# Performance work log

Hardware: AMD Instinct MI355X
Metric: run time of the kernel (lower is better)

## Reference

```python
import jax, jax.numpy as jnp
import numpy as np

B, N, K = 8, 2048, 20
EPS = 1e-5
GROUPS = 32


def setup_inputs() -> dict:
    key = jax.random.key(0)
    ks = jax.random.split(key, 10)
    f32 = jnp.float32
    def W(k_, o, c):
        return jax.random.normal(k_, (o, c), f32) * 0.1
    p = {}
    p["transpose_xyz"] = jax.random.normal(ks[0], (B, 3, N), f32)
    p["w1"] = W(ks[1], 64, 6);    p["g1"] = jnp.ones(64, f32);  p["b1"] = jnp.zeros(64, f32)
    p["w2"] = W(ks[2], 64, 128);  p["g2"] = jnp.ones(64, f32);  p["b2"] = jnp.zeros(64, f32)
    p["w3"] = W(ks[3], 128, 128); p["g3"] = jnp.ones(128, f32); p["b3"] = jnp.zeros(128, f32)
    p["w4"] = W(ks[4], 256, 256); p["g4"] = jnp.ones(256, f32); p["b4"] = jnp.zeros(256, f32)
    p["w5"] = W(ks[5], 512, 512); p["g5"] = jnp.ones(512, f32); p["b5"] = jnp.zeros(512, f32)
    p["wm1"] = W(ks[6], 512, 1536); p["bm1"] = jnp.zeros(512, f32); p["g6"] = jnp.ones(512, f32); p["b6"] = jnp.zeros(512, f32)
    p["wm2"] = W(ks[7], 256, 512);  p["bm2"] = jnp.zeros(256, f32); p["g7"] = jnp.ones(256, f32); p["b7"] = jnp.zeros(256, f32)
    p["wm3"] = W(ks[8], 128, 256);  p["bm3"] = jnp.zeros(128, f32); p["g8"] = jnp.ones(128, f32); p["b8"] = jnp.zeros(128, f32)
    return p


def _lrelu(x):
    return jnp.where(x >= 0, x, 0.2 * x)


def _bn2d(x, g, b):
    # training-mode BatchNorm2d: stats over (B, N, K) per channel, biased variance
    m = jnp.mean(x, axis=(0, 2, 3), keepdims=True)
    v = jnp.var(x, axis=(0, 2, 3), keepdims=True)
    return (x - m) * jax.lax.rsqrt(v + EPS) * g[None, :, None, None] + b[None, :, None, None]


def _gn(x, g, b):
    # GroupNorm over [B, C, L]
    Bx, C, L = x.shape
    xr = x.reshape(Bx, GROUPS, C // GROUPS, L)
    m = jnp.mean(xr, axis=(2, 3), keepdims=True)
    v = jnp.var(xr, axis=(2, 3), keepdims=True)
    xn = ((xr - m) * jax.lax.rsqrt(v + EPS)).reshape(Bx, C, L)
    return xn * g[None, :, None] + b[None, :, None]


def _graph_feature(x, k):
    # x: [B, C, N] -> edge features [B, 2C, N, k]
    xx = jnp.sum(x * x, axis=1)                       # [B, N]
    inner = jnp.einsum('bcn,bcm->bnm', x, x)          # [B, N, N]
    pd = 2.0 * inner - xx[:, :, None] - xx[:, None, :]  # negative sq distance
    idx = jax.lax.top_k(pd, k)[1]                     # [B, N, k] nearest (incl. self)
    xt = jnp.transpose(x, (0, 2, 1))                  # [B, N, C]
    nbr = jax.vmap(lambda a, i: a[i])(xt, idx)        # [B, N, k, C]
    ctr = jnp.broadcast_to(xt[:, :, None, :], nbr.shape)
    f = jnp.concatenate([nbr - ctr, ctr], axis=-1)    # [B, N, k, 2C]
    return jnp.transpose(f, (0, 3, 1, 2))


def _edge_block(x, w, g, b, k):
    f = _graph_feature(x, k)                          # [B, 2C, N, k]
    f = jnp.einsum('oc,bcnk->bonk', w, f)             # 1x1 conv2d, no bias
    f = _lrelu(_bn2d(f, g, b))
    return jnp.max(f, axis=-1)                        # [B, O, N]


def _forward(transpose_xyz, w1, g1, b1, w2, g2, b2, w3, g3, b3, w4, g4, b4,
             w5, g5, b5, wm1, bm1, g6, b6, wm2, bm2, g7, b7, wm3, bm3, g8, b8):
    x1 = _edge_block(transpose_xyz, w1, g1, b1, K)    # [B, 64, N]
    x2 = _edge_block(x1, w2, g2, b2, K)               # [B, 64, N]
    x3 = _edge_block(x2, w3, g3, b3, K)               # [B, 128, N]
    x4 = _edge_block(x3, w4, g4, b4, K)               # [B, 256, N]
    loc = jnp.concatenate([x1, x2, x3, x4], axis=1)   # [B, 512, N]
    h = _lrelu(_gn(jnp.einsum('oc,bcn->bon', w5, loc), g5, b5))  # [B, 512, N]
    glb = jnp.concatenate([jnp.max(h, axis=2), jnp.mean(h, axis=2)], axis=1)  # [B, 1024]
    Bx, _, Nx = loc.shape
    rep = jnp.broadcast_to(glb[:, :, None], (Bx, glb.shape[1], Nx))
    cat = jnp.concatenate([loc, rep], axis=1)         # [B, 1536, N]
    h = jax.nn.relu(_gn(jnp.einsum('oc,bcn->bon', wm1, cat) + bm1[None, :, None], g6, b6))
    h = jax.nn.relu(_gn(jnp.einsum('oc,bcn->bon', wm2, h) + bm2[None, :, None], g7, b7))
    h = jax.nn.relu(_gn(jnp.einsum('oc,bcn->bon', wm3, h) + bm3[None, :, None], g8, b8))
    return h                                          # [B, 128, N]


def reference(transpose_xyz, w1, g1, b1, w2, g2, b2, w3, g3, b3, w4, g4, b4,
              w5, g5, b5, wm1, bm1, g6, b6, wm2, bm2, g7, b7, wm3, bm3, g8, b8):
    return _forward(transpose_xyz, w1, g1, b1, w2, g2, b2, w3, g3, b3, w4, g4, b4,
                    w5, g5, b5, wm1, bm1, g6, b6, wm2, bm2, g7, b7, wm3, bm3, g8, b8)
```

## Files before the change

kernel.cpp:

```cpp
#include <hip/hip_runtime.h>

#define BATCH 8
#define NPTS  2048
#define KNN   20
#define NEG_INF_F (-3.402823466e38f)
#define NEG_INF_D (-1.7976931348623157e308)

__device__ __forceinline__ float fmul_(float a, float b){ return __fmul_rn(a,b); }
__device__ __forceinline__ float fadd_(float a, float b){ return __fadd_rn(a,b); }
__device__ __forceinline__ float fsub_(float a, float b){ return __fsub_rn(a,b); }

__global__ void k_transpose_in(const float* __restrict__ x, float* __restrict__ o) {
    int i = blockIdx.x * blockDim.x + threadIdx.x;
    if (i >= BATCH * 3 * NPTS) return;
    int b = i / (3 * NPTS); int r = i % (3 * NPTS); int c = r / NPTS; int n = r % NPTS;
    size_t row = (size_t)b * NPTS + n;
    o[row * 4 + c] = x[i];
    if (c == 0) o[row * 4 + 3] = 0.f;
}

__global__ void k_sumsq(const float* __restrict__ X, int ldx, int coff, int C,
                        float* __restrict__ xx) {
    int i = blockIdx.x * blockDim.x + threadIdx.x;
    if (i >= BATCH * NPTS) return;
    const float* p = X + (size_t)i * ldx + coff;
    float s = 0.f;
    for (int c = 0; c < C; ++c) s = fadd_(s, fmul_(p[c], p[c]));
    xx[i] = s;
}

__global__ __launch_bounds__(256) void k_pd(const float* __restrict__ Xb, int ldx, int coff, int C,
                                            const float* __restrict__ xxb, float* __restrict__ pd) {
    __shared__ float An[64][17];
    __shared__ float Am[64][17];
    int tx = threadIdx.x, ty = threadIdx.y, tid = ty * 16 + tx;
    int lrow = tid >> 2, lc4 = (tid & 3) << 2;
    int nB = blockIdx.y * 64, mB = blockIdx.x * 64;
    float acc[4][4] = {};
    for (int k0 = 0; k0 < C; k0 += 16) {
        #pragma unroll
        for (int j = 0; j < 4; ++j) {
            int kc = k0 + lc4 + j;
            An[lrow][lc4+j] = (kc < C) ? Xb[(size_t)(nB + lrow) * ldx + coff + kc] : 0.f;
            Am[lrow][lc4+j] = (kc < C) ? Xb[(size_t)(mB + lrow) * ldx + coff + kc] : 0.f;
        }
        __syncthreads();
        #pragma unroll
        for (int kk = 0; kk < 16; ++kk) {
            float a[4], w[4];
            #pragma unroll
            for (int i = 0; i < 4; ++i) a[i] = An[ty*4+i][kk];
            #pragma unroll
            for (int j = 0; j < 4; ++j) w[j] = Am[tx*4+j][kk];
            #pragma unroll
            for (int i = 0; i < 4; ++i)
                #pragma unroll
                for (int j = 0; j < 4; ++j)
                    acc[i][j] = fadd_(acc[i][j], fmul_(a[i], w[j]));
        }
        __syncthreads();
    }
    #pragma unroll
    for (int i = 0; i < 4; ++i) {
        int n = nB + ty*4 + i;
        float xn = xxb[n];
        #pragma unroll
        for (int j = 0; j < 4; ++j) {
            int m = mB + tx*4 + j;
            pd[(size_t)n * NPTS + m] = fsub_(fsub_(fmul_(2.0f, acc[i][j]), xn), xxb[m]);
        }
    }
}

__global__ __launch_bounds__(256) void k_topk(const float* __restrict__ pd, int gbase,
                                              int* __restrict__ idx) {
    __shared__ float wv_[4];
    __shared__ int   wi_[4];
    __shared__ int   gi_;
    int r = blockIdx.x, tid = threadIdx.x;
    const float* src = pd + (size_t)r * NPTS;
    float v[8];
    #pragma unroll
    for (int j = 0; j < 8; ++j) v[j] = src[tid + j * 256];
    float lv = v[0]; int lj = 0;
    #pragma unroll
    for (int j = 1; j < 8; ++j) if (v[j] > lv) { lv = v[j]; lj = j; }
    int lane = tid & 63, wid = tid >> 6;
    for (int it = 0; it < KNN; ++it) {
        float bv = lv; int bm = tid + lj * 256;
        #pragma unroll
        for (int d = 32; d > 0; d >>= 1) {
            float ov = __shfl_xor(bv, d, 64);
            int   om = __shfl_xor(bm, d, 64);
            if (ov > bv || (ov == bv && om < bm)) { bv = ov; bm = om; }
        }
        if (lane == 0) { wv_[wid] = bv; wi_[wid] = bm; }
        __syncthreads();
        if (tid == 0) {
            float gv = wv_[0]; int gm = wi_[0];
            #pragma unroll
            for (int k = 1; k < 4; ++k) {
                float ov = wv_[k]; int om = wi_[k];
                if (ov > gv || (ov == gv && om < gm)) { gv = ov; gm = om; }
            }
            gi_ = gm;
            idx[(size_t)(gbase + r) * KNN + it] = gm;
        }
        __syncthreads();
        int gm = gi_;
        if ((gm & 255) == tid) {
            v[gm >> 8] = NEG_INF_F;
            lv = v[0]; lj = 0;
            #pragma unroll
            for (int j = 1; j < 8; ++j) if (v[j] > lv) { lv = v[j]; lj = j; }
        }
    }
}

#define CCHUNK 16
__global__ void k_edge_conv(const float* __restrict__ X, int ldx, int coff, int C, int O,
                            const float* __restrict__ w, const int* __restrict__ idx,
                            float* __restrict__ ymax, double* __restrict__ part) {
    __shared__ float sc[128];
    __shared__ int   si[KNN];
    __shared__ float sn[KNN * 128];
    __shared__ float wt[256 * (CCHUNK + 1)];
    int o = threadIdx.x;
    int blk = blockIdx.x;
    int C2 = 2 * C;
    double s1 = 0.0, s2 = 0.0;
    for (int jn = 0; jn < 8; ++jn) {
        int n = blk * 8 + jn;
        int b = n >> 11, nl = n & 2047;
        const float* Xb = X + ((size_t)b * NPTS) * ldx + coff;
        for (int t = o; t < C; t += O) sc[t] = Xb[(size_t)nl * ldx + t];
        if (o < KNN) si[o] = idx[(size_t)n * KNN + o];
        __syncthreads();
        for (int t = o; t < KNN * C; t += O) sn[t] = Xb[(size_t)si[t / C] * ldx + (t % C)];
        __syncthreads();
        float acc[KNN];
        #pragma unroll
        for (int k = 0; k < KNN; ++k) acc[k] = 0.f;
        for (int c0 = 0; c0 < C2; c0 += CCHUNK) {
            for (int t = o; t < O * CCHUNK; t += O) {
                int oo = t / CCHUNK, c2 = t % CCHUNK; int c = c0 + c2;
                wt[oo * (CCHUNK + 1) + c2] = (c < C2) ? w[(size_t)oo * C2 + c] : 0.f;
            }
            __syncthreads();
            int cend = (C2 - c0 < CCHUNK) ? (C2 - c0) : CCHUNK;
            for (int c2 = 0; c2 < cend; ++c2) {
                int c = c0 + c2;
                float wv = wt[o * (CCHUNK + 1) + c2];
                if (c < C) {
                    float cv = sc[c];
                    #pragma unroll
                    for (int k = 0; k < KNN; ++k)
                        acc[k] = fadd_(acc[k], fmul_(wv, fsub_(sn[k * C + c], cv)));
                } else {
                    float fv = sc[c - C];
                    #pragma unroll
                    for (int k = 0; k < KNN; ++k)
                        acc[k] = fadd_(acc[k], fmul_(wv, fv));
                }
            }
            __syncthreads();
        }
        float mx = acc[0];
        #pragma unroll
        for (int k = 1; k < KNN; ++k) mx = fmaxf(mx, acc[k]);
        ymax[(size_t)n * O + o] = mx;
        #pragma unroll
        for (int k = 0; k < KNN; ++k) { double v = (double)acc[k]; s1 += v; s2 += v * v; }
        __syncthreads();
    }
    part[(size_t)blk * (2 * O) + o]     = s1;
    part[(size_t)blk * (2 * O) + O + o] = s2;
}

__global__ void k_bn_stats(const double* __restrict__ part, int nparts, int O,
                           float* __restrict__ mst, float* __restrict__ vst) {
    int o = threadIdx.x;
    double s1 = 0.0, s2 = 0.0;
    for (int p = 0; p < nparts; ++p) { s1 += part[(size_t)p * 2 * O + o]; s2 += part[(size_t)p * 2 * O + O + o]; }
    const double cnt = (double)BATCH * NPTS * KNN;
    double m = s1 / cnt;
    double v = s2 / cnt - m * m; if (v < 0.0) v = 0.0;
    mst[o] = (float)m; vst[o] = (float)v;
}

__global__ __launch_bounds__(256) void k_bn_stats4(const double* __restrict__ part, int nparts,
                                                   float* __restrict__ mst, float* __restrict__ vst) {
    __shared__ double r1[256], r2[256];
    int o = blockIdx.x, tid = threadIdx.x;
    double s1 = 0.0, s2 = 0.0;
    for (int p = tid; p < nparts; p += 256) {
        s1 += part[(size_t)p * 512 + o];
        s2 += part[(size_t)p * 512 + 256 + o];
    }
    r1[tid] = s1; r2[tid] = s2;
    __syncthreads();
    for (int s = 128; s > 0; s >>= 1) {
        if (tid < s) { r1[tid] += r1[tid + s]; r2[tid] += r2[tid + s]; }
        __syncthreads();
    }
    if (tid == 0) {
        const double cnt = (double)BATCH * NPTS * KNN;
        double m = r1[0] / cnt;
        double v = r2[0] / cnt - m * m; if (v < 0.0) v = 0.0;
        mst[o] = (float)m; vst[o] = (float)v;
    }
}

__global__ void k_bn_apply(const float* __restrict__ ymax, int O,
                           const float* __restrict__ mst, const float* __restrict__ vst,
                           const float* __restrict__ g, const float* __restrict__ bb,
                           float* __restrict__ loc, int coff) {
    int i = blockIdx.x * blockDim.x + threadIdx.x;
    int m = i / O, o = i % O;
    float r = __fdiv_rn(1.0f, __fsqrt_rn(fadd_(vst[o], 1e-5f)));
    float t = fsub_(ymax[i], mst[o]);
    t = fmul_(t, r);
    t = fmul_(t, g[o]);
    t = fadd_(t, bb[o]);
    if (t < 0.f) t = fmul_(0.2f, t);
    loc[(size_t)m * 512 + coff + o] = t;
}

__global__ void k_wprep(const float* __restrict__ w, int C, int O, float* __restrict__ w2) {
    int i = blockIdx.x * blockDim.x + threadIdx.x;
    if (i >= 2 * O * C) return;
    int o = i / C, c = i % C;
    if (o < O) w2[i] = w[(size_t)o * 2 * C + c];
    else { int oo = o - O; w2[i] = w[(size_t)oo * 2 * C + C + c] - w[(size_t)oo * 2 * C + c]; }
}

__global__ __launch_bounds__(256) void k_gemm_big(const float* __restrict__ A, int lda, int aoff,
                                                  const float* __restrict__ W, int ldw,
                                                  float* __restrict__ out, int ldo, int Kdim,
                                                  const float* __restrict__ bias,
                                                  const double* __restrict__ bvec, int OB,
                                                  size_t zstrA, size_t zstrO) {
    A   += (size_t)blockIdx.z * zstrA;
    out += (size_t)blockIdx.z * zstrO;
    __shared__ float As[128][17];
    __shared__ float Ws[128][17];
    int tx = threadIdx.x, ty = threadIdx.y;
    int tid = ty * 16 + tx;
    int lrow = tid >> 1, kc = (tid & 1) * 8;
    int m0 = blockIdx.y * 128, o0 = blockIdx.x * 128;
    float acc[8][8] = {};
    for (int k0 = 0; k0 < Kdim; k0 += 16) {
        const float* pa = A + (size_t)(m0 + lrow) * lda + aoff + k0 + kc;
        const float* pw = W + (size_t)(o0 + lrow) * ldw + k0 + kc;
        float4 a0 = *(const float4*)pa;
        float4 a1 = *(const float4*)(pa + 4);
        float4 w0 = *(const float4*)pw;
        float4 w1 = *(const float4*)(pw + 4);
        As[lrow][kc+0]=a0.x; As[lrow][kc+1]=a0.y; As[lrow][kc+2]=a0.z; As[lrow][kc+3]=a0.w;
        As[lrow][kc+4]=a1.x; As[lrow][kc+5]=a1.y; As[lrow][kc+6]=a1.z; As[lrow][kc+7]=a1.w;
        Ws[lrow][kc+0]=w0.x; Ws[lrow][kc+1]=w0.y; Ws[lrow][kc+2]=w0.z; Ws[lrow][kc+3]=w0.w;
        Ws[lrow][kc+4]=w1.x; Ws[lrow][kc+5]=w1.y; Ws[lrow][kc+6]=w1.z; Ws[lrow][kc+7]=w1.w;
        __syncthreads();
        #pragma unroll
        for (int kk = 0; kk < 16; ++kk) {
            float a[8], w[8];
            #pragma unroll
            for (int i = 0; i < 8; ++i) a[i] = As[ty*8+i][kk];
            #pragma unroll
            for (int j = 0; j < 8; ++j) w[j] = Ws[tx*8+j][kk];
            #pragma unroll
            for (int i = 0; i < 8; ++i)
                #pragma unroll
                for (int j = 0; j < 8; ++j) acc[i][j] = fmaf(a[i], w[j], acc[i][j]);
        }
        __syncthreads();
    }
    #pragma unroll
    for (int i = 0; i < 8; ++i) {
        int m = m0 + ty*8 + i;
        const double* bv = bvec ? (bvec + (size_t)(m >> 11) * OB) : nullptr;
        #pragma unroll
        for (int j = 0; j < 8; ++j) {
            int o = o0 + tx*8 + j;
            float v = acc[i][j];
            if (bias) v += bias[o];
            if (bv)   v += (float)bv[o];
            out[(size_t)m * ldo + o] = v;
        }
    }
}

__global__ void k_edge_reduce4(const float* __restrict__ zu4, const int* __restrict__ idx,
                               float* __restrict__ ymax, double* __restrict__ part, int b0) {
    __shared__ int sidx[16 * KNN];
    int o = threadIdx.x;
    int tile = blockIdx.x;
    int z = blockIdx.y;
    const float* zu    = zu4  + (size_t)z * NPTS * 512;
    const int*   idxb  = idx  + (size_t)(b0 + z) * NPTS * KNN;
    float*       ymaxb = ymax + (size_t)(b0 + z) * NPTS * 256;
    double*      partb = part + (size_t)(b0 + z) * 128 * 512;
    int n0 = tile * 16;
    for (int t = o; t < 16 * KNN; t += 256)
        sidx[t] = idxb[(size_t)(n0 + t / KNN) * KNN + (t % KNN)];
    __syncthreads();
    double s1 = 0.0, s2 = 0.0;
    for (int nn = 0; nn < 16; ++nn) {
        int n = n0 + nn;
        float u = zu[(size_t)n * 512 + 256 + o];
        float mx = NEG_INF_F; double sz = 0.0, sq = 0.0;
        #pragma unroll
        for (int k = 0; k < KNN; ++k) {
            float zv = zu[(size_t)sidx[nn * KNN + k] * 512 + o];
            mx = fmaxf(mx, zv);
            double y = (double)zv + (double)u;
            sz += (double)zv; sq += y * y;
        }
        ymaxb[(size_t)n * 256 + o] = mx + u;
        s1 += sz + (double)KNN * (double)u;
        s2 += sq;
    }
    partb[(size_t)tile * 512 + o]       = s1;
    partb[(size_t)tile * 512 + 256 + o] = s2;
}

__global__ void k_gn_stats(const float* __restrict__ h, int C, int cg, double* __restrict__ gst) {
    __shared__ double ss[256], sq[256];
    int blk = blockIdx.x;
    int b = blk >> 5, grp = blk & 31;
    int tid = threadIdx.x;
    int tot = NPTS * cg;
    double s = 0.0, q = 0.0;
    for (int e = tid; e < tot; e += 256) {
        int n = e / cg, ci = e % cg;
        double v = (double)h[((size_t)b * NPTS + n) * C + grp * cg + ci];
        s += v; q += v * v;
    }
    ss[tid] = s; sq[tid] = q;
    __syncthreads();
    for (int st = 128; st > 0; st >>= 1) {
        if (tid < st) { ss[tid] += ss[tid + st]; sq[tid] += sq[tid + st]; }
        __syncthreads();
    }
    if (tid == 0) {
        double cnt = (double)tot;
        double mean = ss[0] / cnt;
        double var = fmax(sq[0] / cnt - mean * mean, 0.0);
        gst[blk * 2]     = mean;
        gst[blk * 2 + 1] = rsqrt(var + 1e-5);
    }
}

__global__ void k_gn_apply(float* __restrict__ h, int C, int cg, const double* __restrict__ gst,
                           const float* __restrict__ g, const float* __restrict__ bb, int act) {
    int i = blockIdx.x * blockDim.x + threadIdx.x;
    int m = i / C, c = i % C;
    int b = m >> 11, grp = c / cg;
    double mean = gst[(b * 32 + grp) * 2], inv = gst[(b * 32 + grp) * 2 + 1];
    double v = ((double)h[i] - mean) * inv * (double)g[c] + (double)bb[c];
    v = act ? fmax(v, 0.0) : ((v >= 0.0) ? v : 0.2 * v);
    h[i] = (float)v;
}

__global__ void k_gn_out(const float* __restrict__ h, const double* __restrict__ gst,
                         const float* __restrict__ g, const float* __restrict__ bb,
                         float* __restrict__ out) {
    int i = blockIdx.x * blockDim.x + threadIdx.x;
    int b = i / (128 * NPTS); int r = i % (128 * NPTS); int c = r / NPTS; int n = r % NPTS;
    int grp = c >> 2;
    double mean = gst[(b * 32 + grp) * 2], inv = gst[(b * 32 + grp) * 2 + 1];
    double v = ((double)h[((size_t)b * NPTS + n) * 128 + c] - mean) * inv * (double)g[c] + (double)bb[c];
    out[i] = (float)fmax(v, 0.0);
}

__global__ void k_glb(const float* __restrict__ h, double* __restrict__ glb) {
    __shared__ double smx[256], ssm[256];
    int b  = blockIdx.y;
    int c  = blockIdx.x * 32 + (threadIdx.x & 31);
    int g  = threadIdx.x >> 5;
    const float* hb = h + (size_t)b * NPTS * 512;
    double mx = NEG_INF_D, s = 0.0;
    for (int n = g; n < NPTS; n += 8) {
        double v = (double)hb[(size_t)n * 512 + c];
        mx = fmax(mx, v); s += v;
    }
    smx[threadIdx.x] = mx; ssm[threadIdx.x] = s;
    __syncthreads();
    for (int st = 128; st >= 32; st >>= 1) {
        if (threadIdx.x < st) {
            smx[threadIdx.x] = fmax(smx[threadIdx.x], smx[threadIdx.x + st]);
            ssm[threadIdx.x] += ssm[threadIdx.x + st];
        }
        __syncthreads();
    }
    if (threadIdx.x < 32) {
        glb[b * 1024 + c]       = smx[threadIdx.x];
        glb[b * 1024 + 512 + c] = ssm[threadIdx.x] * (1.0 / NPTS);
    }
}

__global__ void k_vvec(const double* __restrict__ glb, const float* __restrict__ wm1,
                       const float* __restrict__ bm1, double* __restrict__ v) {
    int b = blockIdx.x; int o = threadIdx.x;
    const double* gb = glb + b * 1024;
    const float*  wr = wm1 + (size_t)o * 1536 + 512;
    double s = (double)bm1[o];
    for (int c = 0; c < 1024; ++c) s += gb[c] * (double)wr[c];
    v[b * 512 + o] = s;
}

extern "C" void kernel_launch(void* const* d_in, const int* in_sizes, int n_in,
                              void* d_out, int out_size, void* d_ws, size_t ws_size,
                              hipStream_t stream) {
    const float* xyz = (const float*)d_in[0];
    const float* w1 = (const float*)d_in[1];  const float* g1 = (const float*)d_in[2];  const float* b1 = (const float*)d_in[3];
    const float* w2 = (const float*)d_in[4];  const float* g2 = (const float*)d_in[5];  const float* b2 = (const float*)d_in[6];
    const float* w3 = (const float*)d_in[7];  const float* g3 = (const float*)d_in[8];  const float* b3 = (const float*)d_in[9];
    const float* w4 = (const float*)d_in[10]; const float* g4 = (const float*)d_in[11]; const float* b4 = (const float*)d_in[12];
    const float* w5 = (const float*)d_in[13]; const float* g5 = (const float*)d_in[14]; const float* b5 = (const float*)d_in[15];
    const float* wm1 = (const float*)d_in[16]; const float* bm1 = (const float*)d_in[17];
    const float* g6 = (const float*)d_in[18]; const float* b6 = (const float*)d_in[19];
    const float* wm2 = (const float*)d_in[20]; const float* bm2 = (const float*)d_in[21];
    const float* g7 = (const float*)d_in[22]; const float* b7 = (const float*)d_in[23];
    const float* wm3 = (const float*)d_in[24]; const float* bm3 = (const float*)d_in[25];
    const float* g8 = (const float*)d_in[26]; const float* b8 = (const float*)d_in[27];

    char* ws = (char*)d_ws;
    const size_t MiB = 1024ull * 1024;
    const size_t oLoc  = 0;
    const size_t oU    = 32 * MiB;
    const size_t oPd   = oU;
    const size_t oZu4  = oU;
    const size_t oPart = oU + 16 * MiB;
    const size_t oYmax = oU + 20 * MiB;
    const size_t oH5   = oU;
    const size_t oH7   = oU + 32 * MiB;
    const size_t oX0   = 80 * MiB;
    const size_t oXX   = oX0 + 256 * 1024;
    const size_t oIdx  = oXX + 64 * 1024;
    const size_t oMst  = oIdx + 1344 * 1024;
    const size_t oVst  = oMst + 1024;
    const size_t oGst  = oVst + 1024;
    const size_t oGlb  = oGst + 4096;
    const size_t oVv   = oGlb + 65536;
    const size_t oW2   = oVv + 32768;

    float*  loc  = (float*)(ws + oLoc);
    float*  pd   = (float*)(ws + oPd);
    float*  zu4  = (float*)(ws + oZu4);
    double* part = (double*)(ws + oPart);
    float*  ymax = (float*)(ws + oYmax);
    float*  h5   = (float*)(ws + oH5);
    float*  h7   = (float*)(ws + oH7);
    float*  x0   = (float*)(ws + oX0);
    float*  xx   = (float*)(ws + oXX);
    int*    idx  = (int*)  (ws + oIdx);
    float*  mst  = (float*)(ws + oMst);
    float*  vst  = (float*)(ws + oVst);
    double* gst  = (double*)(ws + oGst);
    double* glb  = (double*)(ws + oGlb);
    double* vv   = (double*)(ws + oVv);
    float*  w2p  = (float*)(ws + oW2);

    dim3 t16(16, 16);
    const int M = BATCH * NPTS;

    k_transpose_in<<<(BATCH*3*NPTS + 255)/256, 256, 0, stream>>>(xyz, x0);

    struct EB { int isX0; int ldx; int coff; int C; int O; const float* w; const float* g; const float* bb; int coff_out; };
    EB eb[3] = {
        { 1, 4,   0,  3,  64,  w1, g1, b1, 0   },
        { 0, 512, 0,  64, 64,  w2, g2, b2, 64  },
        { 0, 512, 64, 64, 128, w3, g3, b3, 128 },
    };
    for (int e = 0; e < 3; ++e) {
        const EB& p = eb[e];
        const float* X = p.isX0 ? x0 : loc;
        k_sumsq<<<M/256, 256, 0, stream>>>(X, p.ldx, p.coff, p.C, xx);
        for (int b = 0; b < BATCH; ++b) {
            k_pd<<<dim3(NPTS/64, NPTS/64), t16, 0, stream>>>(X + (size_t)b*NPTS*p.ldx, p.ldx, p.coff, p.C,
                                                             xx + (size_t)b*NPTS, pd);
            k_topk<<<NPTS, 256, 0, stream>>>(pd, b * NPTS, idx);
        }
        k_edge_conv<<<M/8, p.O, 0, stream>>>(X, p.ldx, p.coff, p.C, p.O, p.w, idx, ymax, part);
        k_bn_stats<<<1, p.O, 0, stream>>>(part, M/8, p.O, mst, vst);
        k_bn_apply<<<(M*p.O)/256, 256, 0, stream>>>(ymax, p.O, mst, vst, p.g, p.bb, loc, p.coff_out);
    }

    k_sumsq<<<M/256, 256, 0, stream>>>(loc, 512, 128, 128, xx);
    for (int b = 0; b < BATCH; ++b) {
        k_pd<<<dim3(NPTS/64, NPTS/64), t16, 0, stream>>>(loc + (size_t)b*NPTS*512, 512, 128, 128,
                                                         xx + (size_t)b*NPTS, pd);
        k_topk<<<NPTS, 256, 0, stream>>>(pd, b * NPTS, idx);
    }
    k_wprep<<<(512*128 + 255)/256, 256, 0, stream>>>(w4, 128, 256, w2p);
    for (int hb = 0; hb < 2; ++hb) {
        int b0 = hb * 4;
        k_gemm_big<<<dim3(512/128, NPTS/128, 4), t16, 0, stream>>>(
            loc + (size_t)b0*NPTS*512, 512, 128, w2p, 128, zu4, 512, 128,
            nullptr, nullptr, 0, (size_t)NPTS*512, (size_t)NPTS*512);
        k_edge_reduce4<<<dim3(128, 4), 256, 0, stream>>>(zu4, idx, ymax, part, b0);
    }
    k_bn_stats4<<<256, 256, 0, stream>>>(part, BATCH*128, mst, vst);
    k_bn_apply<<<(M*256)/256, 256, 0, stream>>>(ymax, 256, mst, vst, g4, b4, loc, 256);

    float* h6 = h5;
    float* h8 = h5;

    k_gemm_big<<<dim3(512/128, M/128), t16, 0, stream>>>(loc, 512, 0, w5, 512, h5, 512, 512,
                                                         nullptr, nullptr, 0, 0, 0);
    k_gn_stats<<<BATCH*32, 256, 0, stream>>>(h5, 512, 16, gst);
    k_gn_apply<<<(M*512)/256, 256, 0, stream>>>(h5, 512, 16, gst, g5, b5, 0);

    k_glb<<<dim3(16, 8), 256, 0, stream>>>(h5, glb);
    k_vvec<<<BATCH, 512, 0, stream>>>(glb, wm1, bm1, vv);

    k_gemm_big<<<dim3(512/128, M/128), t16, 0, stream>>>(loc, 512, 0, wm1, 1536, h6, 512, 512,
                                                         nullptr, vv, 512, 0, 0);
    k_gn_stats<<<BATCH*32, 256, 0, stream>>>(h6, 512, 16, gst);
    k_gn_apply<<<(M*512)/256, 256, 0, stream>>>(h6, 512, 16, gst, g6, b6, 1);

    k_gemm_big<<<dim3(256/128, M/128), t16, 0, stream>>>(h6, 512, 0, wm2, 512, h7, 256, 512,
                                                         bm2, nullptr, 0, 0, 0);
    k_gn_stats<<<BATCH*32, 256, 0, stream>>>(h7, 256, 8, gst);
    k_gn_apply<<<(M*256)/256, 256, 0, stream>>>(h7, 256, 8, gst, g7, b7, 1);

    k_gemm_big<<<dim3(128/128, M/128), t16, 0, stream>>>(h7, 256, 0, wm3, 256, h8, 128, 256,
                                                         bm3, nullptr, 0, 0, 0);
    k_gn_stats<<<BATCH*32, 256, 0, stream>>>(h8, 128, 4, gst);
    k_gn_out<<<(BATCH*128*NPTS)/256, 256, 0, stream>>>(h8, gst, g8, b8, (float*)d_out);
}
```

Before: 6.545 ms.

## Use one wavefront per row in top-k and transpose GEMM shared tiles

The top-k kernel now assigns a single 64-lane wavefront to each distance row, with four rows per block. This removes the per-iteration block barriers and the shared-memory cross-wave reduction; each lane holds 32 values in registers instead of 8. Separately, the GEMM stores its A and W tiles transposed in shared memory, so each thread reads its 8-wide operands with float4 vector loads instead of scalar strided reads. The cost is more registers per lane in top-k and possible bank conflicts on the transposed shared-memory stores.

```diff
diff --git a/kernel.cpp b/kernel.cpp
--- a/kernel.cpp
+++ b/kernel.cpp
@@ -74,45 +74,29 @@
 
 __global__ __launch_bounds__(256) void k_topk(const float* __restrict__ pd, int gbase,
                                               int* __restrict__ idx) {
-    __shared__ float wv_[4];
-    __shared__ int   wi_[4];
-    __shared__ int   gi_;
-    int r = blockIdx.x, tid = threadIdx.x;
+    int wid = threadIdx.x >> 6, lane = threadIdx.x & 63;
+    int r = blockIdx.x * 4 + wid;
     const float* src = pd + (size_t)r * NPTS;
-    float v[8];
+    float v[32];
     #pragma unroll
-    for (int j = 0; j < 8; ++j) v[j] = src[tid + j * 256];
+    for (int j = 0; j < 32; ++j) v[j] = src[lane + j * 64];
     float lv = v[0]; int lj = 0;
     #pragma unroll
-    for (int j = 1; j < 8; ++j) if (v[j] > lv) { lv = v[j]; lj = j; }
-    int lane = tid & 63, wid = tid >> 6;
+    for (int j = 1; j < 32; ++j) if (v[j] > lv) { lv = v[j]; lj = j; }
     for (int it = 0; it < KNN; ++it) {
-        float bv = lv; int bm = tid + lj * 256;
+        float bv = lv; int bm = lane + lj * 64;
         #pragma unroll
         for (int d = 32; d > 0; d >>= 1) {
             float ov = __shfl_xor(bv, d, 64);
             int   om = __shfl_xor(bm, d, 64);
             if (ov > bv || (ov == bv && om < bm)) { bv = ov; bm = om; }
         }
-        if (lane == 0) { wv_[wid] = bv; wi_[wid] = bm; }
-        __syncthreads();
-        if (tid == 0) {
-            float gv = wv_[0]; int gm = wi_[0];
-            #pragma unroll
-            for (int k = 1; k < 4; ++k) {
-                float ov = wv_[k]; int om = wi_[k];
-                if (ov > gv || (ov == gv && om < gm)) { gv = ov; gm = om; }
-            }
-            gi_ = gm;
-            idx[(size_t)(gbase + r) * KNN + it] = gm;
-        }
-        __syncthreads();
-        int gm = gi_;
-        if ((gm & 255) == tid) {
-            v[gm >> 8] = NEG_INF_F;
+        if (lane == 0) idx[(size_t)(gbase + r) * KNN + it] = bm;
+        if ((bm & 63) == lane) {
+            v[bm >> 6] = NEG_INF_F;
             lv = v[0]; lj = 0;
             #pragma unroll
-            for (int j = 1; j < 8; ++j) if (v[j] > lv) { lv = v[j]; lj = j; }
+            for (int j = 1; j < 32; ++j) if (v[j] > lv) { lv = v[j]; lj = j; }
         }
     }
 }
@@ -234,16 +218,16 @@
     else { int oo = o - O; w2[i] = w[(size_t)oo * 2 * C + C + c] - w[(size_t)oo * 2 * C + c]; }
 }
 
-__global__ __launch_bounds__(256) void k_gemm_big(const float* __restrict__ A, int lda, int aoff,
-                                                  const float* __restrict__ W, int ldw,
-                                                  float* __restrict__ out, int ldo, int Kdim,
-                                                  const float* __restrict__ bias,
-                                                  const double* __restrict__ bvec, int OB,
-                                                  size_t zstrA, size_t zstrO) {
+__global__ __launch_bounds__(256) void k_gemm_t(const float* __restrict__ A, int lda, int aoff,
+                                                const float* __restrict__ W, int ldw,
+                                                float* __restrict__ out, int ldo, int Kdim,
+                                                const float* __restrict__ bias,
+                                                const double* __restrict__ bvec, int OB,
+                                                size_t zstrA, size_t zstrO) {
     A   += (size_t)blockIdx.z * zstrA;
     out += (size_t)blockIdx.z * zstrO;
-    __shared__ float As[128][17];
-    __shared__ float Ws[128][17];
+    __shared__ __align__(16) float AsT[16][132];
+    __shared__ __align__(16) float WsT[16][132];
     int tx = threadIdx.x, ty = threadIdx.y;
     int tid = ty * 16 + tx;
     int lrow = tid >> 1, kc = (tid & 1) * 8;
@@ -256,18 +240,19 @@
         float4 a1 = *(const float4*)(pa + 4);
         float4 w0 = *(const float4*)pw;
         float4 w1 = *(const float4*)(pw + 4);
-        As[lrow][kc+0]=a0.x; As[lrow][kc+1]=a0.y; As[lrow][kc+2]=a0.z; As[lrow][kc+3]=a0.w;
-        As[lrow][kc+4]=a1.x; As[lrow][kc+5]=a1.y; As[lrow][kc+6]=a1.z; As[lrow][kc+7]=a1.w;
-        Ws[lrow][kc+0]=w0.x; Ws[lrow][kc+1]=w0.y; Ws[lrow][kc+2]=w0.z; Ws[lrow][kc+3]=w0.w;
-        Ws[lrow][kc+4]=w1.x; Ws[lrow][kc+5]=w1.y; Ws[lrow][kc+6]=w1.z; Ws[lrow][kc+7]=w1.w;
+        AsT[kc+0][lrow]=a0.x; AsT[kc+1][lrow]=a0.y; AsT[kc+2][lrow]=a0.z; AsT[kc+3][lrow]=a0.w;
+        AsT[kc+4][lrow]=a1.x; AsT[kc+5][lrow]=a1.y; AsT[kc+6][lrow]=a1.z; AsT[kc+7][lrow]=a1.w;
+        WsT[kc+0][lrow]=w0.x; WsT[kc+1][lrow]=w0.y; WsT[kc+2][lrow]=w0.z; WsT[kc+3][lrow]=w0.w;
+        WsT[kc+4][lrow]=w1.x; WsT[kc+5][lrow]=w1.y; WsT[kc+6][lrow]=w1.z; WsT[kc+7][lrow]=w1.w;
         __syncthreads();
         #pragma unroll
         for (int kk = 0; kk < 16; ++kk) {
-            float a[8], w[8];
-            #pragma unroll
-            for (int i = 0; i < 8; ++i) a[i] = As[ty*8+i][kk];
-            #pragma unroll
-            for (int j = 0; j < 8; ++j) w[j] = Ws[tx*8+j][kk];
+            float4 aA = *(const float4*)&AsT[kk][ty*8];
+            float4 aB = *(const float4*)&AsT[kk][ty*8+4];
+            float4 wA = *(const float4*)&WsT[kk][tx*8];
+            float4 wB = *(const float4*)&WsT[kk][tx*8+4];
+            float a[8] = {aA.x,aA.y,aA.z,aA.w,aB.x,aB.y,aB.z,aB.w};
+            float w[8] = {wA.x,wA.y,wA.z,wA.w,wB.x,wB.y,wB.z,wB.w};
             #pragma unroll
             for (int i = 0; i < 8; ++i)
                 #pragma unroll
@@ -480,7 +465,7 @@
         for (int b = 0; b < BATCH; ++b) {
             k_pd<<<dim3(NPTS/64, NPTS/64), t16, 0, stream>>>(X + (size_t)b*NPTS*p.ldx, p.ldx, p.coff, p.C,
                                                              xx + (size_t)b*NPTS, pd);
-            k_topk<<<NPTS, 256, 0, stream>>>(pd, b * NPTS, idx);
+            k_topk<<<NPTS/4, 256, 0, stream>>>(pd, b * NPTS, idx);
         }
         k_edge_conv<<<M/8, p.O, 0, stream>>>(X, p.ldx, p.coff, p.C, p.O, p.w, idx, ymax, part);
         k_bn_stats<<<1, p.O, 0, stream>>>(part, M/8, p.O, mst, vst);
@@ -491,12 +476,12 @@
     for (int b = 0; b < BATCH; ++b) {
         k_pd<<<dim3(NPTS/64, NPTS/64), t16, 0, stream>>>(loc + (size_t)b*NPTS*512, 512, 128, 128,
                                                          xx + (size_t)b*NPTS, pd);
-        k_topk<<<NPTS, 256, 0, stream>>>(pd, b * NPTS, idx);
+        k_topk<<<NPTS/4, 256, 0, stream>>>(pd, b * NPTS, idx);
     }
     k_wprep<<<(512*128 + 255)/256, 256, 0, stream>>>(w4, 128, 256, w2p);
     for (int hb = 0; hb < 2; ++hb) {
         int b0 = hb * 4;
-        k_gemm_big<<<dim3(512/128, NPTS/128, 4), t16, 0, stream>>>(
+        k_gemm_t<<<dim3(512/128, NPTS/128, 4), t16, 0, stream>>>(
             loc + (size_t)b0*NPTS*512, 512, 128, w2p, 128, zu4, 512, 128,
             nullptr, nullptr, 0, (size_t)NPTS*512, (size_t)NPTS*512);
         k_edge_reduce4<<<dim3(128, 4), 256, 0, stream>>>(zu4, idx, ymax, part, b0);
@@ -507,26 +492,26 @@
     float* h6 = h5;
     float* h8 = h5;
 
-    k_gemm_big<<<dim3(512/128, M/128), t16, 0, stream>>>(loc, 512, 0, w5, 512, h5, 512, 512,
-                                                         nullptr, nullptr, 0, 0, 0);
+    k_gemm_t<<<dim3(512/128, M/128), t16, 0, stream>>>(loc, 512, 0, w5, 512, h5, 512, 512,
+                                                       nullptr, nullptr, 0, 0, 0);
     k_gn_stats<<<BATCH*32, 256, 0, stream>>>(h5, 512, 16, gst);
     k_gn_apply<<<(M*512)/256, 256, 0, stream>>>(h5, 512, 16, gst, g5, b5, 0);
 
     k_glb<<<dim3(16, 8), 256, 0, stream>>>(h5, glb);
     k_vvec<<<BATCH, 512, 0, stream>>>(glb, wm1, bm1, vv);
 
-    k_gemm_big<<<dim3(512/128, M/128), t16, 0, stream>>>(loc, 512, 0, wm1, 1536, h6, 512, 512,
-                                                         nullptr, vv, 512, 0, 0);
+    k_gemm_t<<<dim3(512/128, M/128), t16, 0, stream>>>(loc, 512, 0, wm1, 1536, h6, 512, 512,
+                                                       nullptr, vv, 512, 0, 0);
     k_gn_stats<<<BATCH*32, 256, 0, stream>>>(h6, 512, 16, gst);
     k_gn_apply<<<(M*512)/256, 256, 0, stream>>>(h6, 512, 16, gst, g6, b6, 1);
 
-    k_gemm_big<<<dim3(256/128, M/128), t16, 0, stream>>>(h6, 512, 0, wm2, 512, h7, 256, 512,
-                                                         bm2, nullptr, 0, 0, 0);
+    k_gemm_t<<<dim3(256/128, M/128), t16, 0, stream>>>(h6, 512, 0, wm2, 512, h7, 256, 512,
+                                                       bm2, nullptr, 0, 0, 0);
     k_gn_stats<<<BATCH*32, 256, 0, stream>>>(h7, 256, 8, gst);
     k_gn_apply<<<(M*256)/256, 256, 0, stream>>>(h7, 256, 8, gst, g7, b7, 1);
 
-    k_gemm_big<<<dim3(128/128, M/128), t16, 0, stream>>>(h7, 256, 0, wm3, 256, h8, 128, 256,
-                                                         bm3, nullptr, 0, 0, 0);
+    k_gemm_t<<<dim3(128/128, M/128), t16, 0, stream>>>(h7, 256, 0, wm3, 256, h8, 128, 256,
+                                                       bm3, nullptr, 0, 0, 0);
     k_gn_stats<<<BATCH*32, 256, 0, stream>>>(h8, 128, 4, gst);
     k_gn_out<<<(BATCH*128*NPTS)/256, 256, 0, stream>>>(h8, gst, g8, b8, (float*)d_out);
 }
```

Measured after the change: 6.102 ms, median of 3. 6.8% less time.
